# Kernel tuning notes

Measured on AMD Instinct MI355X. Metric: run time of the kernel, lower is better.

Reference implementation:

```python
import jax, jax.numpy as jnp
import numpy as np
import math

B, L, S, T = 16, 256, 128, 128
Q_DIM, F_DIM, H_DIM, OUT_DIM = 512, 512, 512, 512


def setup_inputs() -> dict:
    key = jax.random.key(0)
    ks = jax.random.split(key, 10)
    inp = {
        "query": jax.random.normal(ks[0], (B, L, Q_DIM), dtype=jnp.float32),
        "src": jax.random.normal(ks[1], (B, S, F_DIM), dtype=jnp.float32),
        "trg": jax.random.normal(ks[2], (B, T, F_DIM), dtype=jnp.float32),
        # LinearAct params (Linear + identity act; out layer uses tanh)
        "Wq": jax.random.normal(ks[3], (Q_DIM, H_DIM), dtype=jnp.float32) / math.sqrt(Q_DIM),
        "bq": jnp.zeros((H_DIM,), dtype=jnp.float32),
        "Ws": jax.random.normal(ks[4], (F_DIM, H_DIM), dtype=jnp.float32) / math.sqrt(F_DIM),
        "bs": jnp.zeros((H_DIM,), dtype=jnp.float32),
        "Wt": jax.random.normal(ks[5], (F_DIM, H_DIM), dtype=jnp.float32) / math.sqrt(F_DIM),
        "bt": jnp.zeros((H_DIM,), dtype=jnp.float32),
        "Wo": jax.random.normal(ks[6], (2 * H_DIM + Q_DIM, OUT_DIM), dtype=jnp.float32) / math.sqrt(2 * H_DIM + Q_DIM),
        "bo": jnp.zeros((OUT_DIM,), dtype=jnp.float32),
    }
    return inp


def reference(query, src, trg, Wq, bq, Ws, bs, Wt, bt, Wo, bo):
    b, l, _ = query.shape
    _, s, f = src.shape
    _, t, _ = trg.shape
    hid_dim = Wq.shape[1]

    q = query @ Wq + bq                              # b, l, h
    # pad one all-zero feature row onto src and trg (as in torch.cat with pad_tensor)
    pad = jnp.zeros((b, 1, f), dtype=src.dtype)
    src_p = jnp.concatenate([src, pad], axis=1)       # b, s+1, f
    trg_p = jnp.concatenate([trg, pad], axis=1)       # b, t+1, f
    s_key = src_p @ Ws + bs                           # b, s+1, h
    t_key = trg_p @ Wt + bt                           # b, t+1, h

    # trilinear scores: b, l, s+1, t+1
    weight = jnp.einsum('blk,bsk,btk->blst', q, s_key, t_key) / math.sqrt(hid_dim)
    # joint softmax over the flattened (s+1)*(t+1) axis
    weight = jax.nn.softmax(weight.reshape(b, l, -1), axis=-1).reshape(b, l, s + 1, t + 1)

    s_ctx = jnp.einsum('blst,bsk->blk', weight, s_key)  # b, l, h
    t_ctx = jnp.einsum('blst,btk->blk', weight, t_key)  # b, l, h

    x = jnp.concatenate([query, s_ctx, t_ctx], axis=-1)  # b, l, q+2h
    return jnp.tanh(x @ Wo + bo)
```

## Files before the change

### kernel.cpp

```cpp
#include <hip/hip_runtime.h>
#include <math.h>

#define HD 512
#define SP 129
#define RPAD 144
#define WPAD 160
#define NBATCH 16
#define MQ 4096
#define SCALE 0.04419417382415922f
#define SCLG2E 0.06375871645788f
#define TANH2E 2.8853900817779268f

typedef _Float16 f16;
typedef _Float16 f16x8 __attribute__((ext_vector_type(8)));
typedef _Float16 f16x4 __attribute__((ext_vector_type(4)));
typedef float f32x4  __attribute__((ext_vector_type(4)));

__device__ __forceinline__ void gload_lds16(const f16* g, f16* l) {
  __builtin_amdgcn_global_load_lds(
      (const __attribute__((address_space(1))) void*)g,
      (__attribute__((address_space(3))) void*)l, 16, 0, 0);
}

__global__ __launch_bounds__(256) void prep_kernel(
    const float* __restrict__ Wq, const float* __restrict__ Ws,
    const float* __restrict__ Wt, const float* __restrict__ Wo,
    const float* __restrict__ bs, const float* __restrict__ bt,
    f16* __restrict__ WqT, f16* __restrict__ WsT,
    f16* __restrict__ WtT, f16* __restrict__ WoT,
    f16* __restrict__ skey, f16* __restrict__ tkey,
    f16* __restrict__ skeyT, f16* __restrict__ tkeyT)
{
  const int id = blockIdx.x;
  const int tid = threadIdx.x;
  if (id >= 384) {
    int i = (id - 384) * 256 + tid;
    int b = i >> 9, n = i & 511;
    for (int r = 128; r < RPAD; ++r) {
      skey[((size_t)b*RPAD + r)*HD + n] = (r == 128) ? (f16)bs[n] : (f16)0.f;
      tkey[((size_t)b*RPAD + r)*HD + n] = (r == 128) ? (f16)bt[n] : (f16)0.f;
    }
    size_t o = ((size_t)b*512 + n)*WPAD;
    for (int c = 128; c < WPAD; ++c) {
      skeyT[o + c] = (c == 128) ? (f16)bs[n] : (f16)0.f;
      tkeyT[o + c] = (c == 128) ? (f16)bt[n] : (f16)0.f;
    }
    return;
  }
  const float* W; f16* WT; int K; int rest;
  if (id < 64)       { W = Wq; WT = WqT; K = 512;  rest = id; }
  else if (id < 128) { W = Ws; WT = WsT; K = 512;  rest = id - 64; }
  else if (id < 192) { W = Wt; WT = WtT; K = 512;  rest = id - 128; }
  else               { W = Wo; WT = WoT; K = 1536; rest = id - 192; }
  const int k0 = (rest >> 3) * 64, n0 = (rest & 7) * 64;

  __shared__ float t[64][65];
  const int r = tid >> 4, c4 = (tid & 15) * 4;
  #pragma unroll
  for (int i = 0; i < 4; ++i) {
    int k = r + 16*i;
    float4 v = *(const float4*)(W + (size_t)(k0 + k)*512 + n0 + c4);
    t[k][c4] = v.x; t[k][c4+1] = v.y; t[k][c4+2] = v.z; t[k][c4+3] = v.w;
  }
  __syncthreads();
  #pragma unroll
  for (int i = 0; i < 4; ++i) {
    int n = r + 16*i;
    f16x4 v = { (f16)t[c4][n], (f16)t[c4+1][n], (f16)t[c4+2][n], (f16)t[c4+3][n] };
    *(f16x4*)(WT + (size_t)(n0 + n)*K + k0 + c4) = v;
  }
}

__global__ __launch_bounds__(256) void gemm_in(
    const float* __restrict__ query, const float* __restrict__ src,
    const float* __restrict__ trg,
    const f16* __restrict__ WqT, const f16* __restrict__ WsT,
    const f16* __restrict__ WtT,
    const float* __restrict__ bq, const float* __restrict__ bsv,
    const float* __restrict__ btv,
    f16* __restrict__ q_h, f16* __restrict__ skey, f16* __restrict__ tkey,
    f16* __restrict__ skeyT, f16* __restrict__ tkeyT)
{
  __shared__ __align__(16) f16 As[64*64];
  __shared__ __align__(16) f16 Bs[64*64];
  const int x = blockIdx.x;
  const float* A; const f16* WT; const float* bias; int bm; int iskey;
  f16 *Ch, *CT;
  if (x < 64)      { A = query; WT = WqT; bias = bq;  bm = x*64;      iskey = 0; Ch = q_h;  CT = nullptr; }
  else if (x < 96) { A = src;   WT = WsT; bias = bsv; bm = (x-64)*64; iskey = 1; Ch = skey; CT = skeyT; }
  else             { A = trg;   WT = WtT; bias = btv; bm = (x-96)*64; iskey = 1; Ch = tkey; CT = tkeyT; }
  const int bn = blockIdx.y * 64;
  const int tid  = threadIdx.x;
  const int lane = tid & 63;
  const int w    = tid >> 6;
  const int wr   = w & 1, wc = w >> 1;
  const int fq   = lane >> 4, fr = lane & 15;

  f32x4 acc[2][2] = {};

  for (int k0 = 0; k0 < 512; k0 += 64) {
    #pragma unroll
    for (int i = 0; i < 2; ++i) {
      int idx = tid + 256*i;
      int r = idx >> 3, c = idx & 7;
      const float* ap = A + (size_t)(bm + r)*512 + k0 + c*8;
      float4 x0 = *(const float4*)ap;
      float4 x1 = *(const float4*)(ap + 4);
      f16x8 va = { (f16)x0.x, (f16)x0.y, (f16)x0.z, (f16)x0.w,
                   (f16)x1.x, (f16)x1.y, (f16)x1.z, (f16)x1.w };
      const uint4 vb = *(const uint4*)(WT + (size_t)(bn + r)*512 + k0 + c*8);
      int o = ((r << 7) + (c << 4)) ^ ((r & 7) << 4);
      *(f16x8*)((char*)As + o) = va;
      *(uint4*)((char*)Bs + o) = vb;
    }
    __syncthreads();
    #pragma unroll
    for (int ks = 0; ks < 2; ++ks) {
      f16x8 af[2], bf_[2];
      #pragma unroll
      for (int i = 0; i < 2; ++i) {
        int ra = wr*32 + i*16 + fr;
        int oa = ((ra << 7) + (ks << 6) + (fq << 4)) ^ ((ra & 7) << 4);
        af[i] = *(const f16x8*)((const char*)As + oa);
        int rb = wc*32 + i*16 + fr;
        int ob = ((rb << 7) + (ks << 6) + (fq << 4)) ^ ((rb & 7) << 4);
        bf_[i] = *(const f16x8*)((const char*)Bs + ob);
      }
      #pragma unroll
      for (int i = 0; i < 2; ++i)
        #pragma unroll
        for (int j = 0; j < 2; ++j)
          acc[i][j] = __builtin_amdgcn_mfma_f32_16x16x32_f16(af[i], bf_[j], acc[i][j], 0, 0, 0);
    }
    __syncthreads();
  }

  #pragma unroll
  for (int i = 0; i < 2; ++i) {
    #pragma unroll
    for (int j = 0; j < 2; ++j) {
      int n = bn + wc*32 + j*16 + fr;
      float bv = bias[n];
      if (iskey) {
        const int m0 = bm + wr*32 + i*16 + fq*4;
        f16 vals[4];
        #pragma unroll
        for (int r = 0; r < 4; ++r) {
          int m = m0 + r;
          f16 xx = (f16)(acc[i][j][r] + bv);
          vals[r] = xx;
          int mo = (m >> 7) * RPAD + (m & 127);
          Ch[(size_t)mo*512 + n] = xx;
        }
        f16x4 v4 = { vals[0], vals[1], vals[2], vals[3] };
        *(f16x4*)(CT + ((size_t)(m0 >> 7)*512 + n)*WPAD + (m0 & 127)) = v4;
      } else {
        #pragma unroll
        for (int r = 0; r < 4; ++r) {
          int m = bm + wr*32 + i*16 + fq*4 + r;
          Ch[(size_t)m*512 + n] = (f16)(acc[i][j][r] + bv);
        }
      }
    }
  }
}

__global__ __launch_bounds__(256) void border_kernel(
    const f16* __restrict__ q_h, const f16* __restrict__ skey,
    const f16* __restrict__ tkey, float* __restrict__ Sb)
{
  const int blk = blockIdx.x;
  const int b = blk >> 3, z = (blk >> 2) & 1, mt = blk & 3;
  const f16* keys = (z ? skey : tkey) + (size_t)b*RPAD*HD;
  const f16* u    = (z ? tkey : skey) + ((size_t)b*RPAD + 128)*HD;
  const int gid0 = b*256 + mt*64;

  __shared__ __align__(16) f16 Ks[RPAD*32];
  const int tid = threadIdx.x, lane = tid & 63, w = tid >> 6;
  const int fq = lane >> 4, fr = lane & 15;
  const int wslot = ((tid & 3) ^ ((tid >> 3) & 3)) * 8;
  const int rslot = ((fq ^ ((fr >> 1) & 3))) * 8;

  f32x4 acc[9] = {};

  for (int kt = 0; kt < 16; ++kt) {
    uint4 t0, t1, t2;
    {
      int r0 = tid >> 2, c0 = tid & 3;
      t0 = *(const uint4*)(keys + (size_t)r0*HD + kt*32 + c0*8);
      int r1 = (tid + 256) >> 2;
      t1 = *(const uint4*)(keys + (size_t)r1*HD + kt*32 + c0*8);
      if (tid < 64) {
        int r2 = (tid + 512) >> 2;
        t2 = *(const uint4*)(keys + (size_t)r2*HD + kt*32 + c0*8);
      }
    }
    __syncthreads();
    {
      int r0 = tid >> 2;
      *(uint4*)(&Ks[r0*32 + wslot]) = t0;
      int r1 = (tid + 256) >> 2;
      *(uint4*)(&Ks[r1*32 + wslot]) = t1;
      if (tid < 64) {
        int r2 = (tid + 512) >> 2;
        *(uint4*)(&Ks[r2*32 + wslot]) = t2;
      }
    }
    __syncthreads();
    const f16x8 qf = *(const f16x8*)(q_h + (size_t)(gid0 + w*16 + fr)*HD + kt*32 + fq*8);
    const f16x8 uv = *(const f16x8*)(u + kt*32 + fq*8);
    const f16x8 a = qf * uv;
    #pragma unroll
    for (int j = 0; j < 9; ++j) {
      const f16x8 bfr = *(const f16x8*)(&Ks[(j*16 + fr)*32 + rslot]);
      acc[j] = __builtin_amdgcn_mfma_f32_16x16x32_f16(a, bfr, acc[j], 0, 0, 0);
    }
  }

  float* dst = Sb + (size_t)z*MQ*RPAD;
  #pragma unroll
  for (int j = 0; j < 9; ++j)
    #pragma unroll
    for (int r = 0; r < 4; ++r)
      dst[(size_t)(gid0 + w*16 + fq*4 + r)*RPAD + j*16 + fr] = acc[j][r];
}

__global__ __launch_bounds__(256, 4) void attn_core(
    const f16* __restrict__ qg,
    const f16* __restrict__ skey,
    const f16* __restrict__ tkey,
    const float* __restrict__ Sb,
    f16* __restrict__ wsn,
    f16* __restrict__ wtn)
{
  __shared__ __align__(16) f16 KB[2*2*128*32];
  __shared__ __align__(16) f16 qs[HD];
  __shared__ float wsA[2][128];
  __shared__ float wtA[2][128];
  __shared__ float redA[4], redB[4], redC[4], redD[4], redE[4];
  __shared__ float cornerP;

  const int tid  = threadIdx.x;
  const int lane = tid & 63;
  const int w    = tid >> 6;
  const int rb   = w & 1;
  const int cb   = w >> 1;
  const int fq   = lane >> 4;
  const int fr   = lane & 15;
  const int so   = (fq ^ ((fr >> 1) & 3)) << 3;
  const int gc   = ((lane & 3) ^ ((lane >> 3) & 3)) * 8;

  const int gid = ((int)blockIdx.x & 7) * 512 + ((int)blockIdx.x >> 3);
  const int b   = gid >> 8;
  const f16* skg = skey + (size_t)b * RPAD * HD;
  const f16* tkg = tkey + (size_t)b * RPAD * HD;

  if (tid < 64) *(uint4*)(qs + tid*8) = *(const uint4*)(qg + (size_t)gid*HD + tid*8);

  auto stage = [&](int kt, int buf) {
    #pragma unroll
    for (int n = 0; n < 4; ++n) {
      int idx = w*4 + n;
      int key = idx >> 3;
      int rg  = idx & 7;
      const f16* g = (key ? tkg : skg)
                   + (size_t)(rg*16 + (lane >> 2))*HD + kt*32 + gc;
      f16* l = &KB[((buf*2 + key)*128 + rg*16)*32];
      gload_lds16(g, l);
    }
  };

  f32x4 acc[4][4] = {};

  auto mfma_kt = [&](int kt, int cur) {
    const f16x8 qv = *(const f16x8*)(&qs[kt*32 + fq*8]);
    const int abase = (cur*2 + 0)*128*32;
    const int bbase = (cur*2 + 1)*128*32;
    f16x8 B[4];
    #pragma unroll
    for (int j = 0; j < 4; ++j) {
      int rt = cb*64 + j*16 + fr;
      B[j] = *(const f16x8*)(&KB[bbase + rt*32 + so]);
    }
    __builtin_amdgcn_s_setprio(1);
    #pragma unroll
    for (int i = 0; i < 4; ++i) {
      int rs = rb*64 + i*16 + fr;
      const f16x8 raw = *(const f16x8*)(&KB[abase + rs*32 + so]);
      const f16x8 a = raw * qv;
      #pragma unroll
      for (int j = 0; j < 4; ++j)
        acc[i][j] = __builtin_amdgcn_mfma_f32_16x16x32_f16(a, B[j], acc[i][j], 0, 0, 0);
    }
    __builtin_amdgcn_s_setprio(0);
  };

  stage(0, 0);
  __syncthreads();

  for (int kt = 0; kt < 16; ++kt) {
    const int cur = kt & 1;
    if (kt < 15) {
      stage(kt + 1, cur ^ 1);
      asm volatile("s_waitcnt vmcnt(4)" ::: "memory");
    } else {
      asm volatile("s_waitcnt vmcnt(0)" ::: "memory");
    }
    __builtin_amdgcn_s_barrier();
    mfma_kt(kt, cur);
    __builtin_amdgcn_s_barrier();
  }

  float m = -3e38f;
  #pragma unroll
  for (int i = 0; i < 4; ++i)
    #pragma unroll
    for (int j = 0; j < 4; ++j)
      #pragma unroll
      for (int r = 0; r < 4; ++r) m = fmaxf(m, acc[i][j][r]);
  #pragma unroll
  for (int off = 32; off > 0; off >>= 1) m = fmaxf(m, __shfl_xor(m, off));
  if (lane == 0) redA[w] = m;

  const float* SbT = Sb + (size_t)gid*RPAD;
  const float* SbS = Sb + (size_t)MQ*RPAD + (size_t)gid*RPAD;
  const float btv = (tid < 129) ? SbT[tid] : -3e38f;
  const float bsv = (tid < 128) ? SbS[tid] : -3e38f;
  float bm = fmaxf(btv, bsv);
  #pragma unroll
  for (int off = 32; off > 0; off >>= 1) bm = fmaxf(bm, __shfl_xor(bm, off));
  if (lane == 0) redB[w] = bm;
  __syncthreads();
  const float mraw = fmaxf(
      fmaxf(fmaxf(redA[0], redA[1]), fmaxf(redA[2], redA[3])),
      fmaxf(fmaxf(redB[0], redB[1]), fmaxf(redB[2], redB[3])));

  float csum = 0.f;
  #pragma unroll
  for (int i = 0; i < 4; ++i)
    #pragma unroll
    for (int j = 0; j < 4; ++j)
      #pragma unroll
      for (int r = 0; r < 4; ++r) {
        float p = exp2f((acc[i][j][r] - mraw) * SCLG2E);
        acc[i][j][r] = p;
        csum += p;
      }
  #pragma unroll
  for (int off = 32; off > 0; off >>= 1) csum += __shfl_xor(csum, off);
  if (lane == 0) redC[w] = csum;

  #pragma unroll
  for (int i = 0; i < 4; ++i) {
    #pragma unroll
    for (int r = 0; r < 4; ++r) {
      float rs = acc[i][0][r] + acc[i][1][r] + acc[i][2][r] + acc[i][3][r];
      rs += __shfl_xor(rs, 1); rs += __shfl_xor(rs, 2);
      rs += __shfl_xor(rs, 4); rs += __shfl_xor(rs, 8);
      if (fr == 0) wsA[cb][rb*64 + i*16 + fq*4 + r] = rs;
    }
  }
  #pragma unroll
  for (int j = 0; j < 4; ++j) {
    float cs = 0.f;
    #pragma unroll
    for (int i = 0; i < 4; ++i)
      #pragma unroll
      for (int r = 0; r < 4; ++r) cs += acc[i][j][r];
    cs += __shfl_xor(cs, 16); cs += __shfl_xor(cs, 32);
    if (fq == 0) wtA[rb][cb*64 + j*16 + fr] = cs;
  }

  const float pbt = (tid < 129) ? exp2f((btv - mraw) * SCLG2E) : 0.f;
  const float pbs = (tid < 128) ? exp2f((bsv - mraw) * SCLG2E) : 0.f;
  float sbt = pbt, sbs = pbs;
  #pragma unroll
  for (int off = 32; off > 0; off >>= 1) {
    sbt += __shfl_xor(sbt, off);
    sbs += __shfl_xor(sbs, off);
  }
  if (lane == 0) { redD[w] = sbt; redE[w] = sbs; }
  if (tid == 128) cornerP = pbt;
  __syncthreads();

  const float pbt_sum = redD[0] + redD[1] + redD[2] + redD[3];
  const float pbs_sum = redE[0] + redE[1] + redE[2] + redE[3];
  const float core_sum = redC[0] + redC[1] + redC[2] + redC[3];
  const float invZ = 1.0f / (core_sum + pbt_sum + pbs_sum);

  if (tid < WPAD) {
    float wsv = (tid < 128) ? (wsA[0][tid] + wsA[1][tid] + pbs)
              : (tid == 128) ? pbt_sum : 0.f;
    float wtv = (tid < 128) ? (wtA[0][tid] + wtA[1][tid] + pbt)
              : (tid == 128) ? (pbs_sum + cornerP) : 0.f;
    wsn[(size_t)gid*WPAD + tid] = (f16)(wsv * invZ);
    wtn[(size_t)gid*WPAD + tid] = (f16)(wtv * invZ);
  }
}

__global__ __launch_bounds__(256) void ctx_gemm(
    const f16* __restrict__ wsn, const f16* __restrict__ wtn,
    const f16* __restrict__ skeyT, const f16* __restrict__ tkeyT,
    f16* __restrict__ sctx, f16* __restrict__ tctx)
{
  __shared__ __align__(16) f16 As[64*168];
  __shared__ __align__(16) f16 Bs[64*168];
  const int z = blockIdx.x & 1, b = blockIdx.x >> 1;
  const int mt = blockIdx.y, nt = blockIdx.z;
  const int tid = threadIdx.x, lane = tid & 63, w = tid >> 6;
  const int wr = w & 1, wc = w >> 1;
  const int fq = lane >> 4, fr = lane & 15;

  const f16* A  = (z ? wtn : wsn) + ((size_t)b*256 + mt*64)*WPAD;
  const f16* Bt = (z ? tkeyT : skeyT) + ((size_t)b*512 + nt*64)*WPAD;

  for (int t = tid; t < 1280; t += 256) {
    int r = t / 20, c = t % 20;
    *(uint4*)(&As[r*168 + c*8]) = *(const uint4*)(A + (size_t)r*WPAD + c*8);
    *(uint4*)(&Bs[r*168 + c*8]) = *(const uint4*)(Bt + (size_t)r*WPAD + c*8);
  }
  __syncthreads();

  f32x4 acc[2][2] = {};
  #pragma unroll
  for (int ks = 0; ks < 5; ++ks) {
    f16x8 af[2], bf_[2];
    #pragma unroll
    for (int i = 0; i < 2; ++i) {
      af[i]  = *(const f16x8*)(&As[(wr*32 + i*16 + fr)*168 + ks*32 + fq*8]);
      bf_[i] = *(const f16x8*)(&Bs[(wc*32 + i*16 + fr)*168 + ks*32 + fq*8]);
    }
    #pragma unroll
    for (int i = 0; i < 2; ++i)
      #pragma unroll
      for (int j = 0; j < 2; ++j)
        acc[i][j] = __builtin_amdgcn_mfma_f32_16x16x32_f16(af[i], bf_[j], acc[i][j], 0, 0, 0);
  }

  f16* out = z ? tctx : sctx;
  #pragma unroll
  for (int i = 0; i < 2; ++i)
    #pragma unroll
    for (int j = 0; j < 2; ++j) {
      int col = nt*64 + wc*32 + j*16 + fr;
      #pragma unroll
      for (int r = 0; r < 4; ++r) {
        int row = b*256 + mt*64 + wr*32 + i*16 + fq*4 + r;
        out[(size_t)row*HD + col] = (f16)acc[i][j][r];
      }
    }
}

__global__ __launch_bounds__(256) void gemm_out(
    const float* __restrict__ query, const f16* __restrict__ sctx,
    const f16* __restrict__ tctx, const f16* __restrict__ WoT,
    const float* __restrict__ bias, float* __restrict__ C)
{
  __shared__ __align__(16) f16 As[64*64];
  __shared__ __align__(16) f16 Bs[64*64];
  const int tid  = threadIdx.x;
  const int lane = tid & 63;
  const int w    = tid >> 6;
  const int wr   = w & 1, wc = w >> 1;
  const int fq   = lane >> 4, fr = lane & 15;
  const int bm = blockIdx.x * 64, bn = blockIdx.y * 64;

  f32x4 acc[2][2] = {};

  for (int k0 = 0; k0 < 1536; k0 += 64) {
    const int seg  = k0 >> 9;
    const int kloc = k0 & 511;
    #pragma unroll
    for (int i = 0; i < 2; ++i) {
      int idx = tid + 256*i;
      int r = idx >> 3, c = idx & 7;
      int o = ((r << 7) + (c << 4)) ^ ((r & 7) << 4);
      if (seg == 0) {
        const float* ap = query + (size_t)(bm + r)*512 + kloc + c*8;
        float4 x0 = *(const float4*)ap;
        float4 x1 = *(const float4*)(ap + 4);
        f16x8 va = { (f16)x0.x, (f16)x0.y, (f16)x0.z, (f16)x0.w,
                     (f16)x1.x, (f16)x1.y, (f16)x1.z, (f16)x1.w };
        *(f16x8*)((char*)As + o) = va;
      } else {
        const f16* Ap = (seg == 1) ? sctx : tctx;
        *(uint4*)((char*)As + o) = *(const uint4*)(Ap + (size_t)(bm + r)*512 + kloc + c*8);
      }
      *(uint4*)((char*)Bs + o) = *(const uint4*)(WoT + (size_t)(bn + r)*1536 + k0 + c*8);
    }
    __syncthreads();
    #pragma unroll
    for (int ks = 0; ks < 2; ++ks) {
      f16x8 af[2], bf_[2];
      #pragma unroll
      for (int i = 0; i < 2; ++i) {
        int ra = wr*32 + i*16 + fr;
        int oa = ((ra << 7) + (ks << 6) + (fq << 4)) ^ ((ra & 7) << 4);
        af[i] = *(const f16x8*)((const char*)As + oa);
        int rb = wc*32 + i*16 + fr;
        int ob = ((rb << 7) + (ks << 6) + (fq << 4)) ^ ((rb & 7) << 4);
        bf_[i] = *(const f16x8*)((const char*)Bs + ob);
      }
      #pragma unroll
      for (int i = 0; i < 2; ++i)
        #pragma unroll
        for (int j = 0; j < 2; ++j)
          acc[i][j] = __builtin_amdgcn_mfma_f32_16x16x32_f16(af[i], bf_[j], acc[i][j], 0, 0, 0);
    }
    __syncthreads();
  }

  #pragma unroll
  for (int i = 0; i < 2; ++i)
    #pragma unroll
    for (int j = 0; j < 2; ++j) {
      int n = bn + wc*32 + j*16 + fr;
      float bv = bias[n];
      #pragma unroll
      for (int r = 0; r < 4; ++r) {
        int m = bm + wr*32 + i*16 + fq*4 + r;
        float xx = acc[i][j][r] + bv;
        xx = fminf(fmaxf(xx, -20.f), 20.f);
        float e = exp2f(TANH2E * xx);
        C[(size_t)m*HD + n] = (e - 1.0f) / (e + 1.0f);
      }
    }
}

extern "C" void kernel_launch(void* const* d_in, const int* in_sizes, int n_in,
                              void* d_out, int out_size, void* d_ws, size_t ws_size,
                              hipStream_t stream) {
  (void)in_sizes; (void)n_in; (void)out_size; (void)ws_size;
  const float* query = (const float*)d_in[0];
  const float* src   = (const float*)d_in[1];
  const float* trg   = (const float*)d_in[2];
  const float* Wq    = (const float*)d_in[3];
  const float* bq    = (const float*)d_in[4];
  const float* Wsm   = (const float*)d_in[5];
  const float* bs    = (const float*)d_in[6];
  const float* Wtm   = (const float*)d_in[7];
  const float* bt    = (const float*)d_in[8];
  const float* Wo    = (const float*)d_in[9];
  const float* bo    = (const float*)d_in[10];
  float* out = (float*)d_out;

  char* p = (char*)d_ws;
  f16* WqT   = (f16*)p;  p += (size_t)HD*HD*2;
  f16* WsT   = (f16*)p;  p += (size_t)HD*HD*2;
  f16* WtT   = (f16*)p;  p += (size_t)HD*HD*2;
  f16* WoT   = (f16*)p;  p += (size_t)1536*HD*2;
  f16* q_h   = (f16*)p;  p += (size_t)MQ*HD*2;
  f16* skey  = (f16*)p;  p += (size_t)NBATCH*RPAD*HD*2;
  f16* tkey  = (f16*)p;  p += (size_t)NBATCH*RPAD*HD*2;
  f16* skeyT = (f16*)p;  p += (size_t)NBATCH*HD*WPAD*2;
  f16* tkeyT = (f16*)p;  p += (size_t)NBATCH*HD*WPAD*2;
  f16* wsn   = (f16*)p;  p += (size_t)MQ*WPAD*2;
  f16* wtn   = (f16*)p;  p += (size_t)MQ*WPAD*2;
  f16* sctx  = (f16*)p;  p += (size_t)MQ*HD*2;
  f16* tctx  = (f16*)p;  p += (size_t)MQ*HD*2;
  float* Sb  = (float*)p; p += (size_t)2*MQ*RPAD*4;

  dim3 blk(256);
  prep_kernel<<<dim3(416), blk, 0, stream>>>(Wq, Wsm, Wtm, Wo, bs, bt,
                                             WqT, WsT, WtT, WoT,
                                             skey, tkey, skeyT, tkeyT);
  gemm_in<<<dim3(128, 8), blk, 0, stream>>>(query, src, trg, WqT, WsT, WtT,
                                            bq, bs, bt, q_h, skey, tkey,
                                            skeyT, tkeyT);
  border_kernel<<<dim3(128), blk, 0, stream>>>(q_h, skey, tkey, Sb);
  attn_core<<<dim3(MQ), blk, 0, stream>>>(q_h, skey, tkey, Sb, wsn, wtn);
  ctx_gemm<<<dim3(32, 4, 8), blk, 0, stream>>>(wsn, wtn, skeyT, tkeyT, sctx, tctx);
  gemm_out<<<dim3(64, 8), blk, 0, stream>>>(query, sctx, tctx, WoT, bo, out);
}
```

Baseline: 192.9 us.

## Process two query rows per attn_core block with 4-stage K pipeline

Each attn_core block now handles two consecutive query rows, sharing each staged s_key/t_key tile across two accumulator sets and halving the number of blocks. The key staging pipeline grows from double to quadruple buffering with a prefetch distance of two, which drops the trailing barrier per k-step. This is meant to halve global/LDS traffic for key tiles per query and hide more load latency. In exchange register pressure doubles (launch bounds lowered to 2 blocks/CU), LDS use grows, and the two epilogues run serially.

```diff
diff --git a/kernel.cpp b/kernel.cpp
--- a/kernel.cpp
+++ b/kernel.cpp
@@ -225,7 +225,7 @@
       dst[(size_t)(gid0 + w*16 + fq*4 + r)*RPAD + j*16 + fr] = acc[j][r];
 }
 
-__global__ __launch_bounds__(256, 4) void attn_core(
+__global__ __launch_bounds__(256, 2) void attn_core(
     const f16* __restrict__ qg,
     const f16* __restrict__ skey,
     const f16* __restrict__ tkey,
@@ -233,8 +233,8 @@
     f16* __restrict__ wsn,
     f16* __restrict__ wtn)
 {
-  __shared__ __align__(16) f16 KB[2*2*128*32];
-  __shared__ __align__(16) f16 qs[HD];
+  __shared__ __align__(16) f16 KB[4*2*128*32];
+  __shared__ __align__(16) f16 qs[2][HD];
   __shared__ float wsA[2][128];
   __shared__ float wtA[2][128];
   __shared__ float redA[4], redB[4], redC[4], redD[4], redE[4];
@@ -250,12 +250,16 @@
   const int so   = (fq ^ ((fr >> 1) & 3)) << 3;
   const int gc   = ((lane & 3) ^ ((lane >> 3) & 3)) * 8;
 
-  const int gid = ((int)blockIdx.x & 7) * 512 + ((int)blockIdx.x >> 3);
-  const int b   = gid >> 8;
+  const int pair = ((int)blockIdx.x & 7) * 256 + ((int)blockIdx.x >> 3);
+  const int gid0 = pair * 2;
+  const int b    = gid0 >> 8;
   const f16* skg = skey + (size_t)b * RPAD * HD;
   const f16* tkg = tkey + (size_t)b * RPAD * HD;
 
-  if (tid < 64) *(uint4*)(qs + tid*8) = *(const uint4*)(qg + (size_t)gid*HD + tid*8);
+  if (tid < 128) {
+    int row = tid >> 6, n = tid & 63;
+    *(uint4*)(&qs[row][n*8]) = *(const uint4*)(qg + (size_t)(gid0 + row)*HD + n*8);
+  }
 
   auto stage = [&](int kt, int buf) {
     #pragma unroll
@@ -270,12 +274,14 @@
     }
   };
 
-  f32x4 acc[4][4] = {};
-
-  auto mfma_kt = [&](int kt, int cur) {
-    const f16x8 qv = *(const f16x8*)(&qs[kt*32 + fq*8]);
-    const int abase = (cur*2 + 0)*128*32;
-    const int bbase = (cur*2 + 1)*128*32;
+  f32x4 acc0[4][4] = {};
+  f32x4 acc1[4][4] = {};
+
+  auto mfma_kt = [&](int kt, int buf) {
+    const f16x8 qv0 = *(const f16x8*)(&qs[0][kt*32 + fq*8]);
+    const f16x8 qv1 = *(const f16x8*)(&qs[1][kt*32 + fq*8]);
+    const int abase = (buf*2 + 0)*128*32;
+    const int bbase = (buf*2 + 1)*128*32;
     f16x8 B[4];
     #pragma unroll
     for (int j = 0; j < 4; ++j) {
@@ -287,115 +293,126 @@
     for (int i = 0; i < 4; ++i) {
       int rs = rb*64 + i*16 + fr;
       const f16x8 raw = *(const f16x8*)(&KB[abase + rs*32 + so]);
-      const f16x8 a = raw * qv;
+      const f16x8 a0 = raw * qv0;
       #pragma unroll
       for (int j = 0; j < 4; ++j)
-        acc[i][j] = __builtin_amdgcn_mfma_f32_16x16x32_f16(a, B[j], acc[i][j], 0, 0, 0);
+        acc0[i][j] = __builtin_amdgcn_mfma_f32_16x16x32_f16(a0, B[j], acc0[i][j], 0, 0, 0);
+      const f16x8 a1 = raw * qv1;
+      #pragma unroll
+      for (int j = 0; j < 4; ++j)
+        acc1[i][j] = __builtin_amdgcn_mfma_f32_16x16x32_f16(a1, B[j], acc1[i][j], 0, 0, 0);
     }
     __builtin_amdgcn_s_setprio(0);
   };
 
   stage(0, 0);
+  stage(1, 1);
   __syncthreads();
 
   for (int kt = 0; kt < 16; ++kt) {
-    const int cur = kt & 1;
-    if (kt < 15) {
-      stage(kt + 1, cur ^ 1);
+    if (kt < 14) {
+      stage(kt + 2, (kt + 2) & 3);
+      asm volatile("s_waitcnt vmcnt(8)" ::: "memory");
+    } else if (kt == 14) {
       asm volatile("s_waitcnt vmcnt(4)" ::: "memory");
     } else {
       asm volatile("s_waitcnt vmcnt(0)" ::: "memory");
     }
     __builtin_amdgcn_s_barrier();
-    mfma_kt(kt, cur);
-    __builtin_amdgcn_s_barrier();
-  }
-
-  float m = -3e38f;
-  #pragma unroll
-  for (int i = 0; i < 4; ++i)
-    #pragma unroll
-    for (int j = 0; j < 4; ++j)
-      #pragma unroll
-      for (int r = 0; r < 4; ++r) m = fmaxf(m, acc[i][j][r]);
-  #pragma unroll
-  for (int off = 32; off > 0; off >>= 1) m = fmaxf(m, __shfl_xor(m, off));
-  if (lane == 0) redA[w] = m;
-
-  const float* SbT = Sb + (size_t)gid*RPAD;
-  const float* SbS = Sb + (size_t)MQ*RPAD + (size_t)gid*RPAD;
-  const float btv = (tid < 129) ? SbT[tid] : -3e38f;
-  const float bsv = (tid < 128) ? SbS[tid] : -3e38f;
-  float bm = fmaxf(btv, bsv);
-  #pragma unroll
-  for (int off = 32; off > 0; off >>= 1) bm = fmaxf(bm, __shfl_xor(bm, off));
-  if (lane == 0) redB[w] = bm;
+    mfma_kt(kt, kt & 3);
+  }
+
+  auto epilogue = [&](f32x4 (&acc)[4][4], int gid) {
+    float m = -3e38f;
+    #pragma unroll
+    for (int i = 0; i < 4; ++i)
+      #pragma unroll
+      for (int j = 0; j < 4; ++j)
+        #pragma unroll
+        for (int r = 0; r < 4; ++r) m = fmaxf(m, acc[i][j][r]);
+    #pragma unroll
+    for (int off = 32; off > 0; off >>= 1) m = fmaxf(m, __shfl_xor(m, off));
+    if (lane == 0) redA[w] = m;
+
+    const float* SbT = Sb + (size_t)gid*RPAD;
+    const float* SbS = Sb + (size_t)MQ*RPAD + (size_t)gid*RPAD;
+    const float btv = (tid < 129) ? SbT[tid] : -3e38f;
+    const float bsv = (tid < 128) ? SbS[tid] : -3e38f;
+    float bm = fmaxf(btv, bsv);
+    #pragma unroll
+    for (int off = 32; off > 0; off >>= 1) bm = fmaxf(bm, __shfl_xor(bm, off));
+    if (lane == 0) redB[w] = bm;
+    __syncthreads();
+    const float mraw = fmaxf(
+        fmaxf(fmaxf(redA[0], redA[1]), fmaxf(redA[2], redA[3])),
+        fmaxf(fmaxf(redB[0], redB[1]), fmaxf(redB[2], redB[3])));
+
+    float csum = 0.f;
+    #pragma unroll
+    for (int i = 0; i < 4; ++i)
+      #pragma unroll
+      for (int j = 0; j < 4; ++j)
+        #pragma unroll
+        for (int r = 0; r < 4; ++r) {
+          float p = exp2f((acc[i][j][r] - mraw) * SCLG2E);
+          acc[i][j][r] = p;
+          csum += p;
+        }
+    #pragma unroll
+    for (int off = 32; off > 0; off >>= 1) csum += __shfl_xor(csum, off);
+    if (lane == 0) redC[w] = csum;
+
+    #pragma unroll
+    for (int i = 0; i < 4; ++i) {
+      #pragma unroll
+      for (int r = 0; r < 4; ++r) {
+        float rs = acc[i][0][r] + acc[i][1][r] + acc[i][2][r] + acc[i][3][r];
+        rs += __shfl_xor(rs, 1); rs += __shfl_xor(rs, 2);
+        rs += __shfl_xor(rs, 4); rs += __shfl_xor(rs, 8);
+        if (fr == 0) wsA[cb][rb*64 + i*16 + fq*4 + r] = rs;
+      }
+    }
+    #pragma unroll
+    for (int j = 0; j < 4; ++j) {
+      float cs = 0.f;
+      #pragma unroll
+      for (int i = 0; i < 4; ++i)
+        #pragma unroll
+        for (int r = 0; r < 4; ++r) cs += acc[i][j][r];
+      cs += __shfl_xor(cs, 16); cs += __shfl_xor(cs, 32);
+      if (fq == 0) wtA[rb][cb*64 + j*16 + fr] = cs;
+    }
+
+    const float pbt = (tid < 129) ? exp2f((btv - mraw) * SCLG2E) : 0.f;
+    const float pbs = (tid < 128) ? exp2f((bsv - mraw) * SCLG2E) : 0.f;
+    float sbt = pbt, sbs = pbs;
+    #pragma unroll
+    for (int off = 32; off > 0; off >>= 1) {
+      sbt += __shfl_xor(sbt, off);
+      sbs += __shfl_xor(sbs, off);
+    }
+    if (lane == 0) { redD[w] = sbt; redE[w] = sbs; }
+    if (tid == 128) cornerP = pbt;
+    __syncthreads();
+
+    const float pbt_sum = redD[0] + redD[1] + redD[2] + redD[3];
+    const float pbs_sum = redE[0] + redE[1] + redE[2] + redE[3];
+    const float core_sum = redC[0] + redC[1] + redC[2] + redC[3];
+    const float invZ = 1.0f / (core_sum + pbt_sum + pbs_sum);
+
+    if (tid < WPAD) {
+      float wsv = (tid < 128) ? (wsA[0][tid] + wsA[1][tid] + pbs)
+                : (tid == 128) ? pbt_sum : 0.f;
+      float wtv = (tid < 128) ? (wtA[0][tid] + wtA[1][tid] + pbt)
+                : (tid == 128) ? (pbs_sum + cornerP) : 0.f;
+      wsn[(size_t)gid*WPAD + tid] = (f16)(wsv * invZ);
+      wtn[(size_t)gid*WPAD + tid] = (f16)(wtv * invZ);
+    }
+  };
+
+  epilogue(acc0, gid0);
   __syncthreads();
-  const float mraw = fmaxf(
-      fmaxf(fmaxf(redA[0], redA[1]), fmaxf(redA[2], redA[3])),
-      fmaxf(fmaxf(redB[0], redB[1]), fmaxf(redB[2], redB[3])));
-
-  float csum = 0.f;
-  #pragma unroll
-  for (int i = 0; i < 4; ++i)
-    #pragma unroll
-    for (int j = 0; j < 4; ++j)
-      #pragma unroll
-      for (int r = 0; r < 4; ++r) {
-        float p = exp2f((acc[i][j][r] - mraw) * SCLG2E);
-        acc[i][j][r] = p;
-        csum += p;
-      }
-  #pragma unroll
-  for (int off = 32; off > 0; off >>= 1) csum += __shfl_xor(csum, off);
-  if (lane == 0) redC[w] = csum;
-
-  #pragma unroll
-  for (int i = 0; i < 4; ++i) {
-    #pragma unroll
-    for (int r = 0; r < 4; ++r) {
-      float rs = acc[i][0][r] + acc[i][1][r] + acc[i][2][r] + acc[i][3][r];
-      rs += __shfl_xor(rs, 1); rs += __shfl_xor(rs, 2);
-      rs += __shfl_xor(rs, 4); rs += __shfl_xor(rs, 8);
-      if (fr == 0) wsA[cb][rb*64 + i*16 + fq*4 + r] = rs;
-    }
-  }
-  #pragma unroll
-  for (int j = 0; j < 4; ++j) {
-    float cs = 0.f;
-    #pragma unroll
-    for (int i = 0; i < 4; ++i)
-      #pragma unroll
-      for (int r = 0; r < 4; ++r) cs += acc[i][j][r];
-    cs += __shfl_xor(cs, 16); cs += __shfl_xor(cs, 32);
-    if (fq == 0) wtA[rb][cb*64 + j*16 + fr] = cs;
-  }
-
-  const float pbt = (tid < 129) ? exp2f((btv - mraw) * SCLG2E) : 0.f;
-  const float pbs = (tid < 128) ? exp2f((bsv - mraw) * SCLG2E) : 0.f;
-  float sbt = pbt, sbs = pbs;
-  #pragma unroll
-  for (int off = 32; off > 0; off >>= 1) {
-    sbt += __shfl_xor(sbt, off);
-    sbs += __shfl_xor(sbs, off);
-  }
-  if (lane == 0) { redD[w] = sbt; redE[w] = sbs; }
-  if (tid == 128) cornerP = pbt;
-  __syncthreads();
-
-  const float pbt_sum = redD[0] + redD[1] + redD[2] + redD[3];
-  const float pbs_sum = redE[0] + redE[1] + redE[2] + redE[3];
-  const float core_sum = redC[0] + redC[1] + redC[2] + redC[3];
-  const float invZ = 1.0f / (core_sum + pbt_sum + pbs_sum);
-
-  if (tid < WPAD) {
-    float wsv = (tid < 128) ? (wsA[0][tid] + wsA[1][tid] + pbs)
-              : (tid == 128) ? pbt_sum : 0.f;
-    float wtv = (tid < 128) ? (wtA[0][tid] + wtA[1][tid] + pbt)
-              : (tid == 128) ? (pbs_sum + cornerP) : 0.f;
-    wsn[(size_t)gid*WPAD + tid] = (f16)(wsv * invZ);
-    wtn[(size_t)gid*WPAD + tid] = (f16)(wtv * invZ);
-  }
+  epilogue(acc1, gid0 + 1);
 }
 
 __global__ __launch_bounds__(256) void ctx_gemm(
@@ -568,7 +585,7 @@
                                             bq, bs, bt, q_h, skey, tkey,
                                             skeyT, tkeyT);
   border_kernel<<<dim3(128), blk, 0, stream>>>(q_h, skey, tkey, Sb);
-  attn_core<<<dim3(MQ), blk, 0, stream>>>(q_h, skey, tkey, Sb, wsn, wtn);
+  attn_core<<<dim3(MQ/2), blk, 0, stream>>>(q_h, skey, tkey, Sb, wsn, wtn);
   ctx_gemm<<<dim3(32, 4, 8), blk, 0, stream>>>(wsn, wtn, skeyT, tkeyT, sctx, tctx);
   gemm_out<<<dim3(64, 8), blk, 0, stream>>>(query, sctx, tctx, WoT, bo, out);
 }
```

New measurement: 191.8 us. About the same (-0.6%).

## Retile input/output GEMMs to 128x128 with double-buffered LDS and async loads

Applied to the files above, without the earlier changes.

Both the input projection GEMM and the output GEMM move from 64x64 to 128x128 tiles with K-step 32. LDS is double-buffered, and the weight or f16 operand tiles are loaded straight into LDS via global_load_lds. The query is converted to f16 once in a new kernel so gemm_out can stream it asynchronously, and MFMA sections get raised wave priority. This cuts redundant operand traffic and overlaps loads with compute, at the cost of far fewer blocks (256 and 128), which may leave many CUs idle, plus one extra kernel launch.

```diff
diff --git a/kernel.cpp b/kernel.cpp
--- a/kernel.cpp
+++ b/kernel.cpp
@@ -20,6 +20,19 @@
   __builtin_amdgcn_global_load_lds(
       (const __attribute__((address_space(1))) void*)g,
       (__attribute__((address_space(3))) void*)l, 16, 0, 0);
+}
+
+__global__ __launch_bounds__(256) void conv_f32_f16(
+    const float* __restrict__ a, f16* __restrict__ o, int n)
+{
+  int base = (blockIdx.x * 256 + threadIdx.x) * 8;
+  if (base < n) {
+    float4 x = *(const float4*)(a + base);
+    float4 y = *(const float4*)(a + base + 4);
+    f16x8 v = { (f16)x.x, (f16)x.y, (f16)x.z, (f16)x.w,
+                (f16)y.x, (f16)y.y, (f16)y.z, (f16)y.w };
+    *(f16x8*)(o + base) = v;
+  }
 }
 
 __global__ __launch_bounds__(256) void prep_kernel(
@@ -81,68 +94,94 @@
     f16* __restrict__ q_h, f16* __restrict__ skey, f16* __restrict__ tkey,
     f16* __restrict__ skeyT, f16* __restrict__ tkeyT)
 {
-  __shared__ __align__(16) f16 As[64*64];
-  __shared__ __align__(16) f16 Bs[64*64];
+  __shared__ __align__(16) f16 As[2][128*32];
+  __shared__ __align__(16) f16 Bs[2][128*32];
   const int x = blockIdx.x;
-  const float* A; const f16* WT; const float* bias; int bm; int iskey;
+  const int mt = x >> 2, nt = x & 3;
+  const float* A; const f16* WT; const float* bias; int bm, iskey;
   f16 *Ch, *CT;
-  if (x < 64)      { A = query; WT = WqT; bias = bq;  bm = x*64;      iskey = 0; Ch = q_h;  CT = nullptr; }
-  else if (x < 96) { A = src;   WT = WsT; bias = bsv; bm = (x-64)*64; iskey = 1; Ch = skey; CT = skeyT; }
-  else             { A = trg;   WT = WtT; bias = btv; bm = (x-96)*64; iskey = 1; Ch = tkey; CT = tkeyT; }
-  const int bn = blockIdx.y * 64;
+  if (mt < 32)      { A = query; WT = WqT; bias = bq;  bm = mt*128;      iskey = 0; Ch = q_h;  CT = nullptr; }
+  else if (mt < 48) { A = src;   WT = WsT; bias = bsv; bm = (mt-32)*128; iskey = 1; Ch = skey; CT = skeyT; }
+  else              { A = trg;   WT = WtT; bias = btv; bm = (mt-48)*128; iskey = 1; Ch = tkey; CT = tkeyT; }
+  const int bn = nt * 128;
   const int tid  = threadIdx.x;
   const int lane = tid & 63;
   const int w    = tid >> 6;
   const int wr   = w & 1, wc = w >> 1;
   const int fq   = lane >> 4, fr = lane & 15;
-
-  f32x4 acc[2][2] = {};
-
-  for (int k0 = 0; k0 < 512; k0 += 64) {
-    #pragma unroll
-    for (int i = 0; i < 2; ++i) {
-      int idx = tid + 256*i;
-      int r = idx >> 3, c = idx & 7;
-      const float* ap = A + (size_t)(bm + r)*512 + k0 + c*8;
-      float4 x0 = *(const float4*)ap;
-      float4 x1 = *(const float4*)(ap + 4);
-      f16x8 va = { (f16)x0.x, (f16)x0.y, (f16)x0.z, (f16)x0.w,
-                   (f16)x1.x, (f16)x1.y, (f16)x1.z, (f16)x1.w };
-      const uint4 vb = *(const uint4*)(WT + (size_t)(bn + r)*512 + k0 + c*8);
-      int o = ((r << 7) + (c << 4)) ^ ((r & 7) << 4);
-      *(f16x8*)((char*)As + o) = va;
-      *(uint4*)((char*)Bs + o) = vb;
-    }
-    __syncthreads();
-    #pragma unroll
-    for (int ks = 0; ks < 2; ++ks) {
-      f16x8 af[2], bf_[2];
-      #pragma unroll
-      for (int i = 0; i < 2; ++i) {
-        int ra = wr*32 + i*16 + fr;
-        int oa = ((ra << 7) + (ks << 6) + (fq << 4)) ^ ((ra & 7) << 4);
-        af[i] = *(const f16x8*)((const char*)As + oa);
-        int rb = wc*32 + i*16 + fr;
-        int ob = ((rb << 7) + (ks << 6) + (fq << 4)) ^ ((rb & 7) << 4);
-        bf_[i] = *(const f16x8*)((const char*)Bs + ob);
-      }
-      #pragma unroll
-      for (int i = 0; i < 2; ++i)
+  const int so   = (fq ^ ((fr >> 1) & 3)) << 3;
+  const int gc   = ((lane & 3) ^ ((lane >> 3) & 3)) * 8;
+
+  auto stageB = [&](int kt, int buf) {
+    #pragma unroll
+    for (int n = 0; n < 2; ++n) {
+      int rg = w*2 + n;
+      const f16* g = WT + (size_t)(bn + rg*16 + (lane >> 2))*512 + kt*32 + gc;
+      gload_lds16(g, &Bs[buf][rg*16*32]);
+    }
+  };
+  float4 a0[2], a1[2];
+  auto loadA = [&](int kt) {
+    #pragma unroll
+    for (int u = 0; u < 2; ++u) {
+      int t = tid + 256*u;
+      int r = t >> 2, c = t & 3;
+      const float* ap = A + (size_t)(bm + r)*512 + kt*32 + c*8;
+      a0[u] = *(const float4*)ap;
+      a1[u] = *(const float4*)(ap + 4);
+    }
+  };
+  auto writeA = [&](int buf) {
+    #pragma unroll
+    for (int u = 0; u < 2; ++u) {
+      int t = tid + 256*u;
+      int r = t >> 2, c = t & 3;
+      int slot = c ^ ((r >> 1) & 3);
+      f16x8 v = { (f16)a0[u].x, (f16)a0[u].y, (f16)a0[u].z, (f16)a0[u].w,
+                  (f16)a1[u].x, (f16)a1[u].y, (f16)a1[u].z, (f16)a1[u].w };
+      *(f16x8*)(&As[buf][r*32 + slot*8]) = v;
+    }
+  };
+
+  f32x4 acc[4][4] = {};
+
+  stageB(0, 0);
+  loadA(0);
+  writeA(0);
+  __syncthreads();
+
+  for (int kt = 0; kt < 16; ++kt) {
+    const int cur = kt & 1;
+    if (kt < 15) { stageB(kt + 1, cur ^ 1); loadA(kt + 1); }
+    {
+      f16x8 bf_[4];
+      #pragma unroll
+      for (int j = 0; j < 4; ++j)
+        bf_[j] = *(const f16x8*)(&Bs[cur][(wc*64 + j*16 + fr)*32 + so]);
+      __builtin_amdgcn_s_setprio(1);
+      #pragma unroll
+      for (int i = 0; i < 4; ++i) {
+        const f16x8 af = *(const f16x8*)(&As[cur][(wr*64 + i*16 + fr)*32 + so]);
         #pragma unroll
-        for (int j = 0; j < 2; ++j)
-          acc[i][j] = __builtin_amdgcn_mfma_f32_16x16x32_f16(af[i], bf_[j], acc[i][j], 0, 0, 0);
-    }
-    __syncthreads();
-  }
-
-  #pragma unroll
-  for (int i = 0; i < 2; ++i) {
-    #pragma unroll
-    for (int j = 0; j < 2; ++j) {
-      int n = bn + wc*32 + j*16 + fr;
-      float bv = bias[n];
+        for (int j = 0; j < 4; ++j)
+          acc[i][j] = __builtin_amdgcn_mfma_f32_16x16x32_f16(af, bf_[j], acc[i][j], 0, 0, 0);
+      }
+      __builtin_amdgcn_s_setprio(0);
+    }
+    if (kt < 15) {
+      writeA(cur ^ 1);
+      __syncthreads();
+    }
+  }
+
+  #pragma unroll
+  for (int j = 0; j < 4; ++j) {
+    int n = bn + wc*64 + j*16 + fr;
+    float bv = bias[n];
+    #pragma unroll
+    for (int i = 0; i < 4; ++i) {
       if (iskey) {
-        const int m0 = bm + wr*32 + i*16 + fq*4;
+        const int m0 = bm + wr*64 + i*16 + fq*4;
         f16 vals[4];
         #pragma unroll
         for (int r = 0; r < 4; ++r) {
@@ -157,7 +196,7 @@
       } else {
         #pragma unroll
         for (int r = 0; r < 4; ++r) {
-          int m = bm + wr*32 + i*16 + fq*4 + r;
+          int m = bm + wr*64 + i*16 + fq*4 + r;
           Ch[(size_t)m*512 + n] = (f16)(acc[i][j][r] + bv);
         }
       }
@@ -452,79 +491,80 @@
 }
 
 __global__ __launch_bounds__(256) void gemm_out(
-    const float* __restrict__ query, const f16* __restrict__ sctx,
+    const f16* __restrict__ qf16, const f16* __restrict__ sctx,
     const f16* __restrict__ tctx, const f16* __restrict__ WoT,
     const float* __restrict__ bias, float* __restrict__ C)
 {
-  __shared__ __align__(16) f16 As[64*64];
-  __shared__ __align__(16) f16 Bs[64*64];
+  __shared__ __align__(16) f16 As[2][128*32];
+  __shared__ __align__(16) f16 Bs[2][128*32];
+  const int bm = (blockIdx.x >> 2) * 128, bn = (blockIdx.x & 3) * 128;
   const int tid  = threadIdx.x;
   const int lane = tid & 63;
   const int w    = tid >> 6;
   const int wr   = w & 1, wc = w >> 1;
   const int fq   = lane >> 4, fr = lane & 15;
-  const int bm = blockIdx.x * 64, bn = blockIdx.y * 64;
-
-  f32x4 acc[2][2] = {};
-
-  for (int k0 = 0; k0 < 1536; k0 += 64) {
-    const int seg  = k0 >> 9;
-    const int kloc = k0 & 511;
-    #pragma unroll
-    for (int i = 0; i < 2; ++i) {
-      int idx = tid + 256*i;
-      int r = idx >> 3, c = idx & 7;
-      int o = ((r << 7) + (c << 4)) ^ ((r & 7) << 4);
-      if (seg == 0) {
-        const float* ap = query + (size_t)(bm + r)*512 + kloc + c*8;
-        float4 x0 = *(const float4*)ap;
-        float4 x1 = *(const float4*)(ap + 4);
-        f16x8 va = { (f16)x0.x, (f16)x0.y, (f16)x0.z, (f16)x0.w,
-                     (f16)x1.x, (f16)x1.y, (f16)x1.z, (f16)x1.w };
-        *(f16x8*)((char*)As + o) = va;
-      } else {
-        const f16* Ap = (seg == 1) ? sctx : tctx;
-        *(uint4*)((char*)As + o) = *(const uint4*)(Ap + (size_t)(bm + r)*512 + kloc + c*8);
-      }
-      *(uint4*)((char*)Bs + o) = *(const uint4*)(WoT + (size_t)(bn + r)*1536 + k0 + c*8);
-    }
-    __syncthreads();
-    #pragma unroll
-    for (int ks = 0; ks < 2; ++ks) {
-      f16x8 af[2], bf_[2];
-      #pragma unroll
-      for (int i = 0; i < 2; ++i) {
-        int ra = wr*32 + i*16 + fr;
-        int oa = ((ra << 7) + (ks << 6) + (fq << 4)) ^ ((ra & 7) << 4);
-        af[i] = *(const f16x8*)((const char*)As + oa);
-        int rb = wc*32 + i*16 + fr;
-        int ob = ((rb << 7) + (ks << 6) + (fq << 4)) ^ ((rb & 7) << 4);
-        bf_[i] = *(const f16x8*)((const char*)Bs + ob);
-      }
-      #pragma unroll
-      for (int i = 0; i < 2; ++i)
+  const int so   = (fq ^ ((fr >> 1) & 3)) << 3;
+  const int gc   = ((lane & 3) ^ ((lane >> 3) & 3)) * 8;
+
+  auto stage = [&](int kt, int buf) {
+    const int seg = kt >> 4;
+    const f16* Ap = (seg == 0) ? qf16 : (seg == 1) ? sctx : tctx;
+    const int kloc = (kt & 15) * 32;
+    #pragma unroll
+    for (int n = 0; n < 2; ++n) {
+      int rg = w*2 + n;
+      int row = rg*16 + (lane >> 2);
+      gload_lds16(Ap + (size_t)(bm + row)*512 + kloc + gc, &As[buf][rg*16*32]);
+      gload_lds16(WoT + (size_t)(bn + row)*1536 + kt*32 + gc, &Bs[buf][rg*16*32]);
+    }
+  };
+
+  f32x4 acc[4][4] = {};
+
+  stage(0, 0);
+  asm volatile("s_waitcnt vmcnt(0)" ::: "memory");
+  __syncthreads();
+
+  for (int kt = 0; kt < 48; ++kt) {
+    const int cur = kt & 1;
+    if (kt < 47) stage(kt + 1, cur ^ 1);
+    {
+      f16x8 bf_[4];
+      #pragma unroll
+      for (int j = 0; j < 4; ++j)
+        bf_[j] = *(const f16x8*)(&Bs[cur][(wc*64 + j*16 + fr)*32 + so]);
+      __builtin_amdgcn_s_setprio(1);
+      #pragma unroll
+      for (int i = 0; i < 4; ++i) {
+        const f16x8 af = *(const f16x8*)(&As[cur][(wr*64 + i*16 + fr)*32 + so]);
         #pragma unroll
-        for (int j = 0; j < 2; ++j)
-          acc[i][j] = __builtin_amdgcn_mfma_f32_16x16x32_f16(af[i], bf_[j], acc[i][j], 0, 0, 0);
-    }
-    __syncthreads();
-  }
-
-  #pragma unroll
-  for (int i = 0; i < 2; ++i)
-    #pragma unroll
-    for (int j = 0; j < 2; ++j) {
-      int n = bn + wc*32 + j*16 + fr;
-      float bv = bias[n];
+        for (int j = 0; j < 4; ++j)
+          acc[i][j] = __builtin_amdgcn_mfma_f32_16x16x32_f16(af, bf_[j], acc[i][j], 0, 0, 0);
+      }
+      __builtin_amdgcn_s_setprio(0);
+    }
+    if (kt < 47) {
+      asm volatile("s_waitcnt vmcnt(0)" ::: "memory");
+      __syncthreads();
+    }
+  }
+
+  #pragma unroll
+  for (int j = 0; j < 4; ++j) {
+    int n = bn + wc*64 + j*16 + fr;
+    float bv = bias[n];
+    #pragma unroll
+    for (int i = 0; i < 4; ++i) {
       #pragma unroll
       for (int r = 0; r < 4; ++r) {
-        int m = bm + wr*32 + i*16 + fq*4 + r;
+        int m = bm + wr*64 + i*16 + fq*4 + r;
         float xx = acc[i][j][r] + bv;
         xx = fminf(fmaxf(xx, -20.f), 20.f);
         float e = exp2f(TANH2E * xx);
         C[(size_t)m*HD + n] = (e - 1.0f) / (e + 1.0f);
       }
     }
+  }
 }
 
 extern "C" void kernel_launch(void* const* d_in, const int* in_sizes, int n_in,
@@ -550,6 +590,7 @@
   f16* WtT   = (f16*)p;  p += (size_t)HD*HD*2;
   f16* WoT   = (f16*)p;  p += (size_t)1536*HD*2;
   f16* q_h   = (f16*)p;  p += (size_t)MQ*HD*2;
+  f16* qf16  = (f16*)p;  p += (size_t)MQ*HD*2;
   f16* skey  = (f16*)p;  p += (size_t)NBATCH*RPAD*HD*2;
   f16* tkey  = (f16*)p;  p += (size_t)NBATCH*RPAD*HD*2;
   f16* skeyT = (f16*)p;  p += (size_t)NBATCH*HD*WPAD*2;
@@ -564,11 +605,12 @@
   prep_kernel<<<dim3(416), blk, 0, stream>>>(Wq, Wsm, Wtm, Wo, bs, bt,
                                              WqT, WsT, WtT, WoT,
                                              skey, tkey, skeyT, tkeyT);
-  gemm_in<<<dim3(128, 8), blk, 0, stream>>>(query, src, trg, WqT, WsT, WtT,
-                                            bq, bs, bt, q_h, skey, tkey,
-                                            skeyT, tkeyT);
+  conv_f32_f16<<<dim3(MQ*HD/8/256), blk, 0, stream>>>(query, qf16, MQ*HD);
+  gemm_in<<<dim3(256), blk, 0, stream>>>(query, src, trg, WqT, WsT, WtT,
+                                         bq, bs, bt, q_h, skey, tkey,
+                                         skeyT, tkeyT);
   border_kernel<<<dim3(128), blk, 0, stream>>>(q_h, skey, tkey, Sb);
   attn_core<<<dim3(MQ), blk, 0, stream>>>(q_h, skey, tkey, Sb, wsn, wtn);
   ctx_gemm<<<dim3(32, 4, 8), blk, 0, stream>>>(wsn, wtn, skeyT, tkeyT, sctx, tctx);
-  gemm_out<<<dim3(64, 8), blk, 0, stream>>>(query, sctx, tctx, WoT, bo, out);
-}
+  gemm_out<<<dim3(128), blk, 0, stream>>>(qf16, sctx, tctx, WoT, bo, out);
+}
```

Result: slower. 200.4 us (+3.9%).
